# Performance work log

Hardware: AMD Instinct MI355X
Metric: run time of the kernel (lower is better)

The kernel has to match this reference:

```python
import jax, jax.numpy as jnp
from jax import lax
import numpy as np

# Graph / tensor dims
N = 64          # regular nodes (each has a ResistiveTensor state)
N1 = N + 1      # + virtual input node (original node -1), zero state, source-only
E = 513         # 512 random edges + 1 input edge; each edge has its own Reverb conv
B, C, H, W = 8, 3, 64, 64
K = 4           # Reverb kernel_size
EQ = -0.1       # ResistiveTensor equilibrium


def setup_inputs() -> dict:
    key = jax.random.key(0)
    ks = jax.random.split(key, 7)
    states = jax.random.normal(ks[0], (N1, B, C, H, W), jnp.float32)
    states = states.at[N].set(0.0)  # virtual input node has zero state
    noise = jax.random.normal(ks[1], (N1, B, C, H, W), jnp.float32) * 0.05
    conv_w = jax.random.normal(ks[2], (E, C, C, K, K), jnp.float32) * 0.1
    conv_b = jax.random.normal(ks[3], (E, C), jnp.float32) * 0.01
    resistivity = jax.random.uniform(ks[4], (N, B, C, H, W), jnp.float32)
    src = jax.random.randint(ks[5], (E,), 0, N1)   # sources may include input node N
    dst = jax.random.randint(ks[6], (E,), 0, N)    # targets are regular nodes only
    return dict(states=states, noise=noise, conv_w=conv_w, conv_b=conv_b,
                resistivity=resistivity, src=src, dst=dst)


def _conv_same(x, w, b):
    # x: [B,C,H,W], w: [Cout,Cin,K,K]; even kernel -> asymmetric SAME padding (1,2)
    y = lax.conv_general_dilated(x, w, (1, 1), [(1, 2), (1, 2)],
                                 dimension_numbers=('NCHW', 'OIHW', 'NCHW'))
    return y + b[None, :, None, None]


def reference(states, noise, conv_w, conv_b, resistivity, src, dst):
    # Phase 1: per-node activation (with injected noise), as in time_step
    acts = jax.nn.sigmoid(states + noise)            # [N1,B,C,H,W]
    # Phase 2: per-edge gather -> Reverb conv -> scatter-add into target states
    edge_in = acts[src]                              # [E,B,C,H,W] gather
    updates = jax.vmap(_conv_same)(edge_in, conv_w, conv_b)  # [E,B,C,H,W]
    agg = jax.ops.segment_sum(updates, dst, num_segments=N1)  # scatter-add by target
    # ResistiveTensor accumulate: pull toward equilibrium scaled by |resistivity|
    new_states = states + agg
    new_states = new_states.at[:N].add(jnp.abs(resistivity) * (EQ - states[:N]))
    return new_states
```

## Files before the change

kernel.cpp:

```cpp
#include <hip/hip_runtime.h>

#define NN 64
#define BB 8
#define HH 64
#define WW 64
#define EE 513
#define EQF -0.1f
#define IMG 4096
#define CHW 12288

typedef unsigned short u16;
typedef __attribute__((ext_vector_type(8))) short bf16x8;
typedef __attribute__((ext_vector_type(4))) float f32x4;

#define ROWS_P 67
#define B_STR (ROWS_P * 256)
#define N_STR (BB * B_STR)

#define TROW_B 528
#define TILE_B (19 * TROW_B)
#define NPIECE 608

__device__ __forceinline__ u16 f2bf(float f) {
  union { float f; unsigned u; } c; c.f = f;
  return (u16)((c.u + 0x7fffu + ((c.u >> 16) & 1u)) >> 16);
}

__global__ __launch_bounds__(512) void pre_k(const float* __restrict__ conv_w,
                                             const float* __restrict__ conv_b,
                                             const int* __restrict__ src,
                                             const int* __restrict__ dst,
                                             const float* __restrict__ states,
                                             const float* __restrict__ noise,
                                             u16* __restrict__ actsI,
                                             u16* __restrict__ wfrag,
                                             int* __restrict__ csr_off,
                                             int2* __restrict__ csr2,
                                             float* __restrict__ nodeBias,
                                             float* __restrict__ out) {
  __shared__ int sdst[EE];
  __shared__ int ssrc[EE];
  __shared__ int swcnt[8][64];
  __shared__ int spw[8][64];
  __shared__ int soffs[NN + 1];
  __shared__ int slist[EE];
  const int tid = threadIdx.x;
  const int bid = blockIdx.x;

  if (bid == 0) {
    for (int e = tid; e < EE; e += 512) { sdst[e] = dst[e]; ssrc[e] = src[e]; }
    __syncthreads();
    const int wv = tid >> 6, l = tid & 63;
    const int d = sdst[tid];
    int rank = 0, cnt = 0;
    for (int i = 0; i < 64; ++i) {
      int di = __shfl(d, i, 64);
      rank += (di == d && i < l) ? 1 : 0;
      cnt  += (di == l) ? 1 : 0;
    }
    swcnt[wv][l] = cnt;
    __syncthreads();
    if (tid < 64) {
      int s = 0;
      #pragma unroll
      for (int w2 = 0; w2 < 8; ++w2) { spw[w2][tid] = s; s += swcnt[w2][tid]; }
      int tot = s + ((sdst[512] == tid) ? 1 : 0);
      int scan = tot;
      #pragma unroll
      for (int ofs = 1; ofs < 64; ofs <<= 1) {
        int v = __shfl_up(scan, ofs, 64);
        if (tid >= ofs) scan += v;
      }
      soffs[tid] = scan - tot;
      if (tid == 63) soffs[64] = scan;
    }
    __syncthreads();
    slist[soffs[d] + spw[wv][d] + rank] = tid;
    if (tid == 0) { int d5 = sdst[512]; slist[soffs[d5 + 1] - 1] = 512; }
    __syncthreads();
    if (tid <= NN) csr_off[tid] = soffs[tid];
    for (int q = tid; q < EE; q += 512) {
      int ee = slist[q];
      csr2[q] = make_int2(ssrc[ee] * N_STR, ee * 512);
    }
    if (tid < 192) {
      int n = tid / 3, co = tid - n * 3;
      float s = 0.f;
      for (int q = soffs[n]; q < soffs[n + 1]; ++q)
        s += conv_b[slist[q] * 3 + co];
      nodeBias[tid] = s;
    }
  } else if (bid <= 65) {
    int gid = (bid - 1) * 512 + tid;
    if (gid < EE * 64) {
      int e = gid >> 6, l = gid & 63;
      int g = l >> 4, col = l & 15, co = col >> 2, kw = col & 3;
      u16 v[8];
      #pragma unroll
      for (int j = 0; j < 8; ++j) {
        float f = 0.0f;
        if (co < 3 && j < 3) f = conv_w[e * 144 + co * 48 + j * 16 + g * 4 + kw];
        v[j] = f2bf(f);
      }
      uint4 pk;
      pk.x = (unsigned)v[0] | ((unsigned)v[1] << 16);
      pk.y = (unsigned)v[2] | ((unsigned)v[3] << 16);
      pk.z = (unsigned)v[4] | ((unsigned)v[5] << 16);
      pk.w = (unsigned)v[6] | ((unsigned)v[7] << 16);
      *(uint4*)(wfrag + (size_t)gid * 8) = pk;
    }
  } else {
    int idx = (bid - 66) * 512 + tid;
    int w4 = idx & 15, h = (idx >> 4) & 63, b = (idx >> 10) & 7, n = idx >> 13;
    int pbase = (n * 8 + b) * CHW + h * 64 + w4 * 4;
    float4 s0 = *(const float4*)(states + pbase);
    float4 s1 = *(const float4*)(states + pbase + IMG);
    float4 s2 = *(const float4*)(states + pbase + 2 * IMG);
    float4 z0 = *(const float4*)(noise + pbase);
    float4 z1 = *(const float4*)(noise + pbase + IMG);
    float4 z2 = *(const float4*)(noise + pbase + 2 * IMG);
    float a0[4], a1[4], a2[4];
    #pragma unroll
    for (int p = 0; p < 4; ++p) {
      float v0 = ((const float*)&s0)[p] + ((const float*)&z0)[p];
      float v1 = ((const float*)&s1)[p] + ((const float*)&z1)[p];
      float v2 = ((const float*)&s2)[p] + ((const float*)&z2)[p];
      a0[p] = 1.0f / (1.0f + __expf(-v0));
      a1[p] = 1.0f / (1.0f + __expf(-v1));
      a2[p] = 1.0f / (1.0f + __expf(-v2));
    }
    uint4 q0, q1;
    q0.x = (unsigned)f2bf(a0[0]) | ((unsigned)f2bf(a1[0]) << 16);
    q0.y = (unsigned)f2bf(a2[0]);
    q0.z = (unsigned)f2bf(a0[1]) | ((unsigned)f2bf(a1[1]) << 16);
    q0.w = (unsigned)f2bf(a2[1]);
    q1.x = (unsigned)f2bf(a0[2]) | ((unsigned)f2bf(a1[2]) << 16);
    q1.y = (unsigned)f2bf(a2[2]);
    q1.z = (unsigned)f2bf(a0[3]) | ((unsigned)f2bf(a1[3]) << 16);
    q1.w = (unsigned)f2bf(a2[3]);
    u16* dp = actsI + (size_t)((n * 8 + b) * ROWS_P + (h + 1)) * 256 + w4 * 16;
    *(uint4*)dp = q0;
    *(uint4*)(dp + 8) = q1;
    uint4 zz; zz.x = 0u; zz.y = 0u; zz.z = 0u; zz.w = 0u;
    if (h == 0) {
      u16* zp = actsI + (size_t)((n * 8 + b) * ROWS_P + 0) * 256 + w4 * 16;
      *(uint4*)zp = zz; *(uint4*)(zp + 8) = zz;
    }
    if (h == 63) {
      u16* zp = actsI + (size_t)((n * 8 + b) * ROWS_P + 65) * 256 + w4 * 16;
      *(uint4*)zp = zz; *(uint4*)(zp + 8) = zz;
      zp += 256;
      *(uint4*)zp = zz; *(uint4*)(zp + 8) = zz;
    }
    if (n == NN) {
      *(float4*)(out + pbase) = s0;
      *(float4*)(out + pbase + IMG) = s1;
      *(float4*)(out + pbase + 2 * IMG) = s2;
    }
  }
}

__global__ __launch_bounds__(256, 4) void conv_k(const float* __restrict__ states,
                                                 const float* __restrict__ res,
                                                 const u16* __restrict__ actsI,
                                                 const u16* __restrict__ wfrag,
                                                 const int* __restrict__ csr_off,
                                                 const int2* __restrict__ csr2,
                                                 const float* __restrict__ nodeBias,
                                                 float* __restrict__ out) {
  __shared__ __align__(16) char smem[2 * TILE_B];

  const int tid = threadIdx.x, lane = tid & 63, wid = tid >> 6;
  const int bid = blockIdx.x;
  const int ht = bid & 3, b = (bid >> 2) & 7, n = bid >> 5;
  const int R0 = ht * 16;

  int pg[3], pl[3];
  #pragma unroll
  for (int j = 0; j < 3; ++j) {
    int p = tid + j * 256;
    int row = p >> 5, c16 = p & 31;
    pg[j] = b * B_STR + (R0 + row) * 256 + c16 * 8;
    pl[j] = row * TROW_B + c16 * 16;
  }
  const bool pv2 = (tid + 512) < NPIECE;

  const int g = lane >> 4, px = lane & 15;
  const int abase = (wid * 4 + g) * TROW_B + px * 8;

  f32x4 acc[4][4];
  #pragma unroll
  for (int wr = 0; wr < 4; ++wr)
    #pragma unroll
    for (int t = 0; t < 4; ++t) { acc[wr][t][0]=0.f; acc[wr][t][1]=0.f; acc[wr][t][2]=0.f; acc[wr][t][3]=0.f; }

  const int e0 = csr_off[n], cnt = csr_off[n + 1] - e0;

  uint4 a0, a1, a2; bf16x8 wa;
  uint4 b0, b1, b2; bf16x8 wb;

#define LOADP(R0_,R1_,R2_,WF_,I_) do {                                        \
    int2 c_ = csr2[e0 + (I_)];                                                \
    int sx_ = __builtin_amdgcn_readfirstlane(c_.x);                           \
    int wx_ = __builtin_amdgcn_readfirstlane(c_.y);                           \
    const u16* ap_ = actsI + sx_;                                             \
    R0_ = *(const uint4*)(ap_ + pg[0]);                                       \
    R1_ = *(const uint4*)(ap_ + pg[1]);                                       \
    if (pv2) R2_ = *(const uint4*)(ap_ + pg[2]);                              \
    WF_ = *(const bf16x8*)(wfrag + wx_ + lane * 8);                           \
  } while (0)

#define STOREP(R0_,R1_,R2_,BUF_) do {                                         \
    *(uint4*)(smem + (BUF_) + pl[0]) = R0_;                                   \
    *(uint4*)(smem + (BUF_) + pl[1]) = R1_;                                   \
    if (pv2) *(uint4*)(smem + (BUF_) + pl[2]) = R2_;                          \
  } while (0)

#define COMP(BUF_,WF_) do {                                                   \
    _Pragma("unroll")                                                         \
    for (int wr_ = 0; wr_ < 4; ++wr_) {                                       \
      _Pragma("unroll")                                                       \
      for (int t_ = 0; t_ < 4; ++t_) {                                        \
        short4 d_ = *(const short4*)(smem + (BUF_) + abase + wr_ * TROW_B + t_ * 128); \
        bf16x8 av_;                                                           \
        av_[0]=d_.x; av_[1]=d_.y; av_[2]=d_.z; av_[3]=d_.w;                   \
        av_[4]=0; av_[5]=0; av_[6]=0; av_[7]=0;                               \
        acc[wr_][t_] = __builtin_amdgcn_mfma_f32_16x16x32_bf16(av_, WF_, acc[wr_][t_], 0, 0, 0); \
      }                                                                       \
    }                                                                         \
  } while (0)

  if (cnt > 0) LOADP(a0, a1, a2, wa, 0);
  if (cnt > 1) LOADP(b0, b1, b2, wb, 1);
  for (int i = 0; i < cnt; i += 2) {
    STOREP(a0, a1, a2, 0);
    bf16x8 wca = wa;
    __syncthreads();
    if (i + 2 < cnt) LOADP(a0, a1, a2, wa, i + 2);
    COMP(0, wca);
    if (i + 1 < cnt) {
      STOREP(b0, b1, b2, TILE_B);
      bf16x8 wcb = wb;
      __syncthreads();
      if (i + 3 < cnt) LOADP(b0, b1, b2, wb, i + 3);
      COMP(TILE_B, wcb);
    }
  }

  __syncthreads();
  float* zr = (float*)(smem + wid * 3328);
  const float bc0 = nodeBias[n * 3 + 0];
  const float bc1 = nodeBias[n * 3 + 1];
  const float bc2 = nodeBias[n * 3 + 2];
  const int col = lane & 15;
  #pragma unroll
  for (int wr = 0; wr < 4; ++wr) {
    if (col < 12) {
      #pragma unroll
      for (int t = 0; t < 4; ++t)
        #pragma unroll
        for (int r = 0; r < 4; ++r)
          zr[(t * 16 + g * 4 + r) * 13 + col] = acc[wr][t][r];
    }
    int hr = R0 + wid * 4 + wr;
    #pragma unroll
    for (int co = 0; co < 3; ++co) {
      float y = (co == 0) ? bc0 : ((co == 1) ? bc1 : bc2);
      #pragma unroll
      for (int kw = 0; kw < 4; ++kw) {
        int wp = lane + kw - 1;
        if (wp >= 0 && wp < 64) y += zr[wp * 13 + co * 4 + kw];
      }
      int o = ((n * 8 + b) * 3 + co) * IMG + hr * 64 + lane;
      float st = states[o];
      out[o] = st + fabsf(res[o]) * (EQF - st) + y;
    }
  }
}

extern "C" void kernel_launch(void* const* d_in, const int* in_sizes, int n_in,
                              void* d_out, int out_size, void* d_ws, size_t ws_size,
                              hipStream_t stream) {
  const float* states = (const float*)d_in[0];
  const float* noise  = (const float*)d_in[1];
  const float* conv_w = (const float*)d_in[2];
  const float* conv_b = (const float*)d_in[3];
  const float* res    = (const float*)d_in[4];
  const int*   src    = (const int*)d_in[5];
  const int*   dst    = (const int*)d_in[6];
  float* out = (float*)d_out;

  u16* actsI = (u16*)d_ws;
  u16* wfrag = (u16*)((char*)d_ws + 17838080);
  int* csr_off = (int*)((char*)d_ws + 18363392);
  int2* csr2 = (int2*)((char*)d_ws + 18363712);
  float* nodeBias = (float*)((char*)d_ws + 18367816);

  pre_k<<<1106, 512, 0, stream>>>(conv_w, conv_b, src, dst, states, noise,
                                  actsI, wfrag, csr_off, csr2, nodeBias, out);
  conv_k<<<2048, 256, 0, stream>>>(states, res, actsI, wfrag, csr_off, csr2, nodeBias, out);
}
```

Before: 53.80 us.

## Deepen edge prefetch to three register sets with custom barrier and node-major block order

The conv kernel now keeps three in-flight edge tile loads in registers instead of two, rotating through them while still double-buffering LDS with an XOR offset. Barriers are replaced by a custom s_waitcnt lgkmcnt(0)+s_barrier that does not wait on outstanding global loads, so prefetches can stay in flight across the barrier. Block index decoding is reordered so adjacent blocks cover different nodes, which changes L2 sharing of activations and the load balance across edge counts. The extra register set raises VGPR pressure and may hurt occupancy under the 256x4 launch bounds.

```diff
diff --git a/kernel.cpp b/kernel.cpp
--- a/kernel.cpp
+++ b/kernel.cpp
@@ -24,6 +24,11 @@
 __device__ __forceinline__ u16 f2bf(float f) {
   union { float f; unsigned u; } c; c.f = f;
   return (u16)((c.u + 0x7fffu + ((c.u >> 16) & 1u)) >> 16);
+}
+
+__device__ __forceinline__ void wg_barrier() {
+  asm volatile("s_waitcnt lgkmcnt(0)\n\ts_barrier" ::: "memory");
+  __builtin_amdgcn_sched_barrier(0);
 }
 
 __global__ __launch_bounds__(512) void pre_k(const float* __restrict__ conv_w,
@@ -172,7 +177,7 @@
 
   const int tid = threadIdx.x, lane = tid & 63, wid = tid >> 6;
   const int bid = blockIdx.x;
-  const int ht = bid & 3, b = (bid >> 2) & 7, n = bid >> 5;
+  const int n = bid & 63, ht = (bid >> 6) & 3, b = (bid >> 8) & 7;
   const int R0 = ht * 16;
 
   int pg[3], pl[3];
@@ -198,6 +203,7 @@
 
   uint4 a0, a1, a2; bf16x8 wa;
   uint4 b0, b1, b2; bf16x8 wb;
+  uint4 c0, c1, c2; bf16x8 wc;
 
 #define LOADP(R0_,R1_,R2_,WF_,I_) do {                                        \
     int2 c_ = csr2[e0 + (I_)];                                                \
@@ -210,18 +216,18 @@
     WF_ = *(const bf16x8*)(wfrag + wx_ + lane * 8);                           \
   } while (0)
 
-#define STOREP(R0_,R1_,R2_,BUF_) do {                                         \
-    *(uint4*)(smem + (BUF_) + pl[0]) = R0_;                                   \
-    *(uint4*)(smem + (BUF_) + pl[1]) = R1_;                                   \
-    if (pv2) *(uint4*)(smem + (BUF_) + pl[2]) = R2_;                          \
+#define STOREP(R0_,R1_,R2_,BOFS_) do {                                        \
+    *(uint4*)(smem + (BOFS_) + pl[0]) = R0_;                                  \
+    *(uint4*)(smem + (BOFS_) + pl[1]) = R1_;                                  \
+    if (pv2) *(uint4*)(smem + (BOFS_) + pl[2]) = R2_;                         \
   } while (0)
 
-#define COMP(BUF_,WF_) do {                                                   \
+#define COMP(BOFS_,WF_) do {                                                  \
     _Pragma("unroll")                                                         \
     for (int wr_ = 0; wr_ < 4; ++wr_) {                                       \
       _Pragma("unroll")                                                       \
       for (int t_ = 0; t_ < 4; ++t_) {                                        \
-        short4 d_ = *(const short4*)(smem + (BUF_) + abase + wr_ * TROW_B + t_ * 128); \
+        short4 d_ = *(const short4*)(smem + (BOFS_) + abase + wr_ * TROW_B + t_ * 128); \
         bf16x8 av_;                                                           \
         av_[0]=d_.x; av_[1]=d_.y; av_[2]=d_.z; av_[3]=d_.w;                   \
         av_[4]=0; av_[5]=0; av_[6]=0; av_[7]=0;                               \
@@ -230,22 +236,27 @@
     }                                                                         \
   } while (0)
 
+#define PHASE(R0_,R1_,R2_,WF_,NEXTI_) do {                                    \
+    STOREP(R0_, R1_, R2_, bofs);                                              \
+    bf16x8 wcur_ = WF_;                                                       \
+    if ((NEXTI_) < cnt) LOADP(R0_, R1_, R2_, WF_, (NEXTI_));                  \
+    wg_barrier();                                                             \
+    COMP(bofs, wcur_);                                                        \
+    bofs ^= TILE_B;                                                           \
+  } while (0)
+
   if (cnt > 0) LOADP(a0, a1, a2, wa, 0);
   if (cnt > 1) LOADP(b0, b1, b2, wb, 1);
-  for (int i = 0; i < cnt; i += 2) {
-    STOREP(a0, a1, a2, 0);
-    bf16x8 wca = wa;
-    __syncthreads();
-    if (i + 2 < cnt) LOADP(a0, a1, a2, wa, i + 2);
-    COMP(0, wca);
-    if (i + 1 < cnt) {
-      STOREP(b0, b1, b2, TILE_B);
-      bf16x8 wcb = wb;
-      __syncthreads();
-      if (i + 3 < cnt) LOADP(b0, b1, b2, wb, i + 3);
-      COMP(TILE_B, wcb);
-    }
+  if (cnt > 2) LOADP(c0, c1, c2, wc, 2);
+  int bofs = 0;
+  int i = 0;
+  for (; i + 2 < cnt; i += 3) {
+    PHASE(a0, a1, a2, wa, i + 3);
+    PHASE(b0, b1, b2, wb, i + 4);
+    PHASE(c0, c1, c2, wc, i + 5);
   }
+  if (i < cnt)     PHASE(a0, a1, a2, wa, cnt);
+  if (i + 1 < cnt) PHASE(b0, b1, b2, wb, cnt);
 
   __syncthreads();
   float* zr = (float*)(smem + wid * 3328);
```

Result: slower. 76.05 us (+41.4%).
